# Optimization experiments

Hardware: AMD Instinct MI355X
Metric: run time of the kernel (lower is better)

Reference implementation:

```python
import jax, jax.numpy as jnp
import numpy as np

B, N, DIM, EMB_H, EXP, K = 1, 1024, 64, 64, 4, 16


def setup_inputs() -> dict:
    key = jax.random.key(0)
    ks = jax.random.split(key, 12)
    s = lambda k, *shape: jax.random.normal(k, shape, dtype=jnp.float32) * 0.05
    return {
        "x": jax.random.normal(ks[0], (B, N, DIM), dtype=jnp.float32),
        "pos": jax.random.normal(ks[1], (B, N, 3), dtype=jnp.float32),
        "Wq": s(ks[2], DIM, DIM),
        "Wk": s(ks[3], DIM, DIM),
        "Wv": s(ks[4], DIM, DIM),
        "P1": s(ks[5], 3, EMB_H), "pb1": jnp.zeros((EMB_H,), jnp.float32),
        "P2": s(ks[6], EMB_H, DIM), "pb2": jnp.zeros((DIM,), jnp.float32),
        "A1": s(ks[7], DIM, DIM * EXP), "ab1": jnp.zeros((DIM * EXP,), jnp.float32),
        "A2": s(ks[8], DIM * EXP, DIM), "ab2": jnp.zeros((DIM,), jnp.float32),
        "nneighbors": K,
    }


def reference(x, pos, Wq, Wk, Wv, P1, pb1, P2, pb2, A1, ab1, A2, ab2, nneighbors):
    b, n, d = x.shape
    q = x @ Wq            # [b,n,d]
    k = x @ Wk
    v = x @ Wv
    qk_rel = q[:, :, None, :] - k[:, None, :, :]          # [b,n,n,d]
    rel_pos = pos[:, :, None, :] - pos[:, None, :, :]      # [b,n,n,3]
    rel_pos_emb = jax.nn.relu(rel_pos @ P1 + pb1) @ P2 + pb2  # [b,n,n,d]
    # kNN selection on euclidean distance (smallest nneighbors)
    rel_dist = jnp.linalg.norm(rel_pos, axis=-1)           # [b,n,n]
    _, idx = jax.lax.top_k(-rel_dist, nneighbors)          # [b,n,K]
    bidx = jnp.arange(b)[:, None, None]
    v_g = v[bidx, idx]                                     # [b,n,K,d]
    qk_g = jnp.take_along_axis(qk_rel, idx[..., None], axis=2)        # [b,n,K,d]
    rpe_g = jnp.take_along_axis(rel_pos_emb, idx[..., None], axis=2)  # [b,n,K,d]
    v_g = v_g + rpe_g
    sim = jax.nn.relu((qk_g + rpe_g) @ A1 + ab1) @ A2 + ab2  # [b,n,K,d]
    attn = jax.nn.softmax(sim, axis=-2)                      # softmax over neighbors
    agg = jnp.sum(attn * v_g, axis=2)                        # [b,n,d]
    return agg
```

## Files before the change

kernel.cpp:

```cpp
#include <hip/hip_runtime.h>
#include <climits>

#define NPTS 1024
#define DIMD 64
#define KNN  16
#define HID  256
#define EMBH 64

typedef short short8 __attribute__((ext_vector_type(8)));
typedef float f32x4  __attribute__((ext_vector_type(4)));

__device__ __forceinline__ short f2bf(float x) {
    unsigned u = __float_as_uint(x);
    unsigned r = (u + 0x7fffu + ((u >> 16) & 1u)) >> 16;
    return (short)r;
}
__device__ __forceinline__ float bf2f(short s) {
    return __uint_as_float(((unsigned)(unsigned short)s) << 16);
}

#define AOFF(k, m) ((((k) >> 3) * 16 + (m)) * 8 + ((k) & 7))

#define A1H 0
#define A2H 16384
#define WKH 32768
#define WVH 36864
#define P2H 40960

__global__ __launch_bounds__(256) void prep_weights(
    const float* __restrict__ A1, const float* __restrict__ A2,
    const float* __restrict__ Wk, const float* __restrict__ Wv,
    const float* __restrict__ P2, short* __restrict__ ws)
{
    int e = blockIdx.x * 256 + threadIdx.x;
    if (e >= 88 * 64) return;
    int f = e >> 6, lane = e & 63;
    int q = (lane >> 4) & 3, nn = lane & 15;
    const float* src; int N, base, lf, cpt;
    if (f < 32)      { src = A1; N = 256; base = A1H; lf = f;      cpt = 2; }
    else if (f < 64) { src = A2; N = 64;  base = A2H; lf = f - 32; cpt = 8; }
    else if (f < 72) { src = Wk; N = 64;  base = WKH; lf = f - 64; cpt = 2; }
    else if (f < 80) { src = Wv; N = 64;  base = WVH; lf = f - 72; cpt = 2; }
    else             { src = P2; N = 64;  base = P2H; lf = f - 80; cpt = 2; }
    int T = lf / cpt, c = lf % cpt;
    int n  = T * 16 + nn;
    int k0 = c * 32 + q * 8;
    short8 v;
    #pragma unroll
    for (int j = 0; j < 8; j++) v[j] = f2bf(src[(k0 + j) * N + n]);
    *(short8*)(ws + base + lf * 512 + lane * 8) = v;
}

__global__ __launch_bounds__(256, 4) void ptl_fused(
    const float* __restrict__ x,  const float* __restrict__ pos,
    const float* __restrict__ Wq,
    const float* __restrict__ P1, const float* __restrict__ pb1,
    const float* __restrict__ pb2,
    const float* __restrict__ ab1, const float* __restrict__ ab2,
    const short* __restrict__ ws,
    float* __restrict__ out)
{
    __shared__ __align__(16) short a_xn_hi[16*64],  a_xn_lo[16*64];
    __shared__ __align__(16) short a_es_hi[16*64],  a_es_lo[16*64];
    __shared__ __align__(16) short a_h_hi [16*64],  a_h_lo [16*64];
    __shared__ __align__(16) short a_hd[2*16*256];
    __shared__ __align__(16) float s_vg[16*68];
    __shared__ __align__(16) float s_sim[16*68];
    __shared__ float s_q[DIMD];
    __shared__ int   s_idx[KNN];
    __shared__ int   s_cnt, s_cnt2, s_need;
    __shared__ unsigned s_pref;

    short* a_hd_hi = a_hd;
    short* a_hd_lo = a_hd + 16*256;

    const int i    = blockIdx.x;
    const int tid  = threadIdx.x;
    const int lane = tid & 63;
    const int w    = tid >> 6;
    const int q4   = lane >> 4;
    const int col  = lane & 15;

    const float px = pos[i*3+0], py = pos[i*3+1], pz = pos[i*3+2];

    unsigned ku[4];
    #pragma unroll
    for (int u = 0; u < 4; u++) {
        int j = tid + 256 * u;
        float dx = __fsub_rn(px, pos[j*3+0]);
        float dy = __fsub_rn(py, pos[j*3+1]);
        float dz = __fsub_rn(pz, pos[j*3+2]);
        float s  = __fadd_rn(__fadd_rn(__fmul_rn(dx,dx), __fmul_rn(dy,dy)), __fmul_rn(dz,dz));
        ku[u] = __float_as_uint(__fsqrt_rn(s));
    }

    int* histI = (int*)a_hd;
    int* s_tie = (int*)(a_hd + 16*256);
    const int g = w * 4 + q4;
    if (tid == 0) { s_cnt = 0; s_cnt2 = 0; s_pref = 0u; s_need = KNN; }

    for (int r = 0; r < 4; r++) {
        const int shift = 24 - 8 * r;
        for (int t = tid; t < 16 * 256; t += 256) histI[t] = 0;
        __syncthreads();
        unsigned pref = s_pref;
        #pragma unroll
        for (int u = 0; u < 4; u++) {
            unsigned k = ku[u];
            bool match = true;
            if (r > 0) match = ((k >> (shift + 8)) == (pref >> (shift + 8)));
            if (match) atomicAdd(&histI[g * 256 + ((k >> shift) & 255)], 1);
        }
        __syncthreads();
        if (w == 0) {
            int b0 = lane * 4, cnt4[4], loc = 0;
            #pragma unroll
            for (int t = 0; t < 4; t++) {
                int s = 0;
                #pragma unroll
                for (int gg = 0; gg < 16; gg++) s += histI[gg * 256 + b0 + t];
                cnt4[t] = s; loc += s;
            }
            int incl = loc;
            #pragma unroll
            for (int off = 1; off < 64; off <<= 1) {
                int t = __shfl_up(incl, off);
                if (lane >= off) incl += t;
            }
            int excl = incl - loc;
            int need = s_need;
            unsigned long long mk = __ballot(incl >= need);
            int lstar = (int)__ffsll((long long)mk) - 1;
            if (lane == lstar) {
                int run = excl, t = 0;
                while (t < 3 && run + cnt4[t] < need) { run += cnt4[t]; t++; }
                s_pref = pref | ((unsigned)(b0 + t) << shift);
                s_need = need - run;
            }
        }
        __syncthreads();
    }
    const unsigned T = s_pref;
    const int needT  = s_need;

    #pragma unroll
    for (int u = 0; u < 4; u++) {
        unsigned k = ku[u];
        int j = tid + 256 * u;
        if (k < T)       { int p = atomicAdd(&s_cnt, 1);  s_idx[p] = j; }
        else if (k == T) { int p = atomicAdd(&s_cnt2, 1); if (p < 256) s_tie[p] = j; }
    }
    __syncthreads();

    if (w == 0) {
        int base = s_cnt;
        int m = s_cnt2;
        if (m == needT) {
            for (int t = lane; t < m; t += 64) s_idx[base + t] = s_tie[t];
        } else {
            int cand[4];
            #pragma unroll
            for (int t = 0; t < 4; t++) {
                int e = lane + 64 * t;
                cand[t] = (e < m && e < 256) ? s_tie[e] : INT_MAX;
            }
            for (int sel = 0; sel < needT; sel++) {
                int mv = cand[0];
                #pragma unroll
                for (int t = 1; t < 4; t++) mv = min(mv, cand[t]);
                #pragma unroll
                for (int off = 32; off > 0; off >>= 1) mv = min(mv, __shfl_xor(mv, off));
                #pragma unroll
                for (int t = 0; t < 4; t++) if (cand[t] == mv) cand[t] = INT_MAX;
                if (lane == 0) s_idx[base + sel] = mv;
            }
        }
    } else if (w == 1) {
        int d = lane;
        const float4* xr = (const float4*)(x + i * DIMD);
        float aq = 0.f;
        #pragma unroll
        for (int cb = 0; cb < DIMD / 4; cb++) {
            float4 xv = xr[cb];
            const float* wq = Wq + (cb*4) * DIMD + d;
            aq = fmaf(xv.x, wq[0*DIMD], aq); aq = fmaf(xv.y, wq[1*DIMD], aq);
            aq = fmaf(xv.z, wq[2*DIMD], aq); aq = fmaf(xv.w, wq[3*DIMD], aq);
        }
        s_q[d] = aq;
    }
    __syncthreads();

    #pragma unroll
    for (int u = 0; u < 4; u++) {
        int t = tid + 256 * u;
        int kk = t >> 6, c = t & 63;
        int j = s_idx[kk];
        int ao = AOFF(c, kk);
        float xv = x[j * DIMD + c];
        short xh = f2bf(xv);
        a_xn_hi[ao] = xh;
        a_xn_lo[ao] = f2bf(xv - bf2f(xh));
        float dx = px - pos[j*3+0];
        float dy = py - pos[j*3+1];
        float dz = pz - pos[j*3+2];
        float a = pb1[c];
        a = fmaf(dx, P1[0*EMBH+c], a);
        a = fmaf(dy, P1[1*EMBH+c], a);
        a = fmaf(dz, P1[2*EMBH+c], a);
        a = fmaxf(a, 0.0f);
        short eh = f2bf(a);
        a_es_hi[ao] = eh;
        a_es_lo[ao] = f2bf(a - bf2f(eh));
    }
    __syncthreads();

    const short8* wsv  = (const short8*)ws;
    const short8* xnh  = (const short8*)a_xn_hi;
    const short8* xnl  = (const short8*)a_xn_lo;
    const short8* esh  = (const short8*)a_es_hi;
    const short8* esl  = (const short8*)a_es_lo;
    const short8* hhv  = (const short8*)a_h_hi;
    const short8* hlv  = (const short8*)a_h_lo;
    const short8* hdh  = (const short8*)a_hd_hi;
    const short8* hdl  = (const short8*)a_hd_lo;

    auto bfrag = [&](int short_base, int f) -> short8 {
        return wsv[(short_base >> 3) + f * 64 + lane];
    };

    {
        f32x4 acck = {0,0,0,0}, accv = {0,0,0,0}, accr = {0,0,0,0};
        #pragma unroll
        for (int c = 0; c < 2; c++) {
            int av = (4*c + q4) * 16 + col;
            short8 xh = xnh[av], xl = xnl[av];
            int f = w * 2 + c;
            short8 bk = bfrag(WKH, f);
            short8 bv = bfrag(WVH, f);
            acck = __builtin_amdgcn_mfma_f32_16x16x32_bf16(xh, bk, acck, 0,0,0);
            acck = __builtin_amdgcn_mfma_f32_16x16x32_bf16(xl, bk, acck, 0,0,0);
            accv = __builtin_amdgcn_mfma_f32_16x16x32_bf16(xh, bv, accv, 0,0,0);
            accv = __builtin_amdgcn_mfma_f32_16x16x32_bf16(xl, bv, accv, 0,0,0);
        }
        #pragma unroll
        for (int c = 0; c < 2; c++) {
            int av = (4*c + q4) * 16 + col;
            short8 eh = esh[av], el = esl[av];
            short8 bp = bfrag(P2H, w * 2 + c);
            accr = __builtin_amdgcn_mfma_f32_16x16x32_bf16(eh, bp, accr, 0,0,0);
            accr = __builtin_amdgcn_mfma_f32_16x16x32_bf16(el, bp, accr, 0,0,0);
        }
        int d = w * 16 + col;
        float qd = s_q[d], pb = pb2[d];
        #pragma unroll
        for (int r = 0; r < 4; r++) {
            int s = q4 * 4 + r;
            float rpe = accr[r] + pb;
            float hv  = qd - acck[r] + rpe;
            s_vg[s * 68 + d] = accv[r] + rpe;
            int ao = AOFF(d, s);
            short hh = f2bf(hv);
            a_h_hi[ao] = hh;
            a_h_lo[ao] = f2bf(hv - bf2f(hh));
        }
    }
    __syncthreads();

    {
        short8 hh[2], hl[2];
        #pragma unroll
        for (int c = 0; c < 2; c++) {
            int av = (4*c + q4) * 16 + col;
            hh[c] = hhv[av]; hl[c] = hlv[av];
        }
        #pragma unroll
        for (int t = 0; t < 4; t++) {
            int T4 = w * 4 + t;
            f32x4 acc = {0,0,0,0};
            #pragma unroll
            for (int c = 0; c < 2; c++) {
                short8 bh = bfrag(A1H, T4 * 2 + c);
                acc = __builtin_amdgcn_mfma_f32_16x16x32_bf16(hh[c], bh, acc, 0,0,0);
                acc = __builtin_amdgcn_mfma_f32_16x16x32_bf16(hl[c], bh, acc, 0,0,0);
            }
            int n = T4 * 16 + col;
            float bias = ab1[n];
            #pragma unroll
            for (int r = 0; r < 4; r++) {
                float val = fmaxf(acc[r] + bias, 0.0f);
                int ao = AOFF(n, q4 * 4 + r);
                short vh = f2bf(val);
                a_hd_hi[ao] = vh;
                a_hd_lo[ao] = f2bf(val - bf2f(vh));
            }
        }
    }
    __syncthreads();

    {
        f32x4 acc0 = {0,0,0,0}, acc1 = {0,0,0,0};
        #pragma unroll
        for (int c = 0; c < 8; c += 2) {
            {
                int av = (4*c + q4) * 16 + col;
                short8 ah = hdh[av], al = hdl[av];
                short8 bh = bfrag(A2H, w * 8 + c);
                acc0 = __builtin_amdgcn_mfma_f32_16x16x32_bf16(ah, bh, acc0, 0,0,0);
                acc0 = __builtin_amdgcn_mfma_f32_16x16x32_bf16(al, bh, acc0, 0,0,0);
            }
            {
                int av = (4*(c+1) + q4) * 16 + col;
                short8 ah = hdh[av], al = hdl[av];
                short8 bh = bfrag(A2H, w * 8 + c + 1);
                acc1 = __builtin_amdgcn_mfma_f32_16x16x32_bf16(ah, bh, acc1, 0,0,0);
                acc1 = __builtin_amdgcn_mfma_f32_16x16x32_bf16(al, bh, acc1, 0,0,0);
            }
        }
        int n = w * 16 + col;
        float bias = ab2[n];
        #pragma unroll
        for (int r = 0; r < 4; r++)
            s_sim[(q4 * 4 + r) * 68 + n] = acc0[r] + acc1[r] + bias;
    }
    __syncthreads();

    if (tid < DIMD) {
        int d = tid;
        float mx = -3.0e38f;
        #pragma unroll
        for (int kk = 0; kk < KNN; kk++) mx = fmaxf(mx, s_sim[kk * 68 + d]);
        float den = 0.0f, num = 0.0f;
        #pragma unroll
        for (int kk = 0; kk < KNN; kk++) {
            float e = expf(s_sim[kk * 68 + d] - mx);
            den += e;
            num = fmaf(e, s_vg[kk * 68 + d], num);
        }
        out[i * DIMD + d] = num / den;
    }
}

extern "C" void kernel_launch(void* const* d_in, const int* in_sizes, int n_in,
                              void* d_out, int out_size, void* d_ws, size_t ws_size,
                              hipStream_t stream) {
    const float* x   = (const float*)d_in[0];
    const float* pos = (const float*)d_in[1];
    const float* Wq  = (const float*)d_in[2];
    const float* Wk  = (const float*)d_in[3];
    const float* Wv  = (const float*)d_in[4];
    const float* P1  = (const float*)d_in[5];
    const float* pb1 = (const float*)d_in[6];
    const float* P2  = (const float*)d_in[7];
    const float* pb2 = (const float*)d_in[8];
    const float* A1  = (const float*)d_in[9];
    const float* ab1 = (const float*)d_in[10];
    const float* A2  = (const float*)d_in[11];
    const float* ab2 = (const float*)d_in[12];
    float* out = (float*)d_out;
    short* ws  = (short*)d_ws;

    prep_weights<<<22, 256, 0, stream>>>(A1, A2, Wk, Wv, P2, ws);
    ptl_fused<<<NPTS, 256, 0, stream>>>(x, pos, Wq, P1, pb1, pb2, ab1, ab2, ws, out);
}
```

Measured before the change: 97.36 us.

## Drop bf16 hi/lo split and redo radix-select with per-wave double-buffered histograms

Activations are now rounded once to bf16 instead of being split into hi and lo parts, which halves the MFMA count and the LDS traffic for the A operands in every GEMM stage. The kNN radix select now uses four per-wave histograms in double-buffered LDS. Every wave does the scan redundantly and shares prefix and need through shuffles instead of shared variables, which removes one barrier per round and the full histogram clear. The cost is lower activation precision, so outputs may drift further from the fp32 reference.

```diff
diff --git a/kernel.cpp b/kernel.cpp
--- a/kernel.cpp
+++ b/kernel.cpp
@@ -14,9 +14,6 @@
     unsigned u = __float_as_uint(x);
     unsigned r = (u + 0x7fffu + ((u >> 16) & 1u)) >> 16;
     return (short)r;
-}
-__device__ __forceinline__ float bf2f(short s) {
-    return __uint_as_float(((unsigned)(unsigned short)s) << 16);
 }
 
 #define AOFF(k, m) ((((k) >> 3) * 16 + (m)) * 8 + ((k) & 7))
@@ -60,19 +57,17 @@
     const short* __restrict__ ws,
     float* __restrict__ out)
 {
-    __shared__ __align__(16) short a_xn_hi[16*64],  a_xn_lo[16*64];
-    __shared__ __align__(16) short a_es_hi[16*64],  a_es_lo[16*64];
-    __shared__ __align__(16) short a_h_hi [16*64],  a_h_lo [16*64];
-    __shared__ __align__(16) short a_hd[2*16*256];
+    __shared__ __align__(16) short a_xn[16*64];
+    __shared__ __align__(16) short a_es[16*64];
+    __shared__ __align__(16) short a_h [16*64];
+    __shared__ __align__(16) short a_hd[16*256];
     __shared__ __align__(16) float s_vg[16*68];
     __shared__ __align__(16) float s_sim[16*68];
     __shared__ float s_q[DIMD];
+    __shared__ int   s_hist[2 * 1028];
+    __shared__ int   s_tie[256];
     __shared__ int   s_idx[KNN];
-    __shared__ int   s_cnt, s_cnt2, s_need;
-    __shared__ unsigned s_pref;
-
-    short* a_hd_hi = a_hd;
-    short* a_hd_lo = a_hd + 16*256;
+    __shared__ int   s_cnt, s_cnt2;
 
     const int i    = blockIdx.x;
     const int tid  = threadIdx.x;
@@ -80,6 +75,9 @@
     const int w    = tid >> 6;
     const int q4   = lane >> 4;
     const int col  = lane & 15;
+
+    int* histA = s_hist;
+    int* histB = s_hist + 1028;
 
     const float px = pos[i*3+0], py = pos[i*3+1], pz = pos[i*3+2];
 
@@ -93,55 +91,51 @@
         float s  = __fadd_rn(__fadd_rn(__fmul_rn(dx,dx), __fmul_rn(dy,dy)), __fmul_rn(dz,dz));
         ku[u] = __float_as_uint(__fsqrt_rn(s));
     }
-
-    int* histI = (int*)a_hd;
-    int* s_tie = (int*)(a_hd + 16*256);
-    const int g = w * 4 + q4;
-    if (tid == 0) { s_cnt = 0; s_cnt2 = 0; s_pref = 0u; s_need = KNN; }
-
+    if (tid == 0) { s_cnt = 0; s_cnt2 = 0; }
+    for (int t = lane; t < 257; t += 64) { histA[w*257 + t] = 0; histB[w*257 + t] = 0; }
+    __syncthreads();
+
+    unsigned pref = 0u; int need = KNN;
     for (int r = 0; r < 4; r++) {
         const int shift = 24 - 8 * r;
-        for (int t = tid; t < 16 * 256; t += 256) histI[t] = 0;
-        __syncthreads();
-        unsigned pref = s_pref;
+        int* cur = (r & 1) ? histB : histA;
         #pragma unroll
         for (int u = 0; u < 4; u++) {
             unsigned k = ku[u];
-            bool match = true;
-            if (r > 0) match = ((k >> (shift + 8)) == (pref >> (shift + 8)));
-            if (match) atomicAdd(&histI[g * 256 + ((k >> shift) & 255)], 1);
+            bool match = (r == 0) || ((k >> (shift + 8)) == (pref >> (shift + 8)));
+            if (match) atomicAdd(&cur[w * 257 + ((k >> shift) & 255)], 1);
         }
         __syncthreads();
-        if (w == 0) {
-            int b0 = lane * 4, cnt4[4], loc = 0;
+        int b0 = lane * 4, cnt4[4], loc = 0;
+        #pragma unroll
+        for (int t = 0; t < 4; t++) {
+            int s = 0;
             #pragma unroll
-            for (int t = 0; t < 4; t++) {
-                int s = 0;
-                #pragma unroll
-                for (int gg = 0; gg < 16; gg++) s += histI[gg * 256 + b0 + t];
-                cnt4[t] = s; loc += s;
-            }
-            int incl = loc;
-            #pragma unroll
-            for (int off = 1; off < 64; off <<= 1) {
-                int t = __shfl_up(incl, off);
-                if (lane >= off) incl += t;
-            }
-            int excl = incl - loc;
-            int need = s_need;
-            unsigned long long mk = __ballot(incl >= need);
-            int lstar = (int)__ffsll((long long)mk) - 1;
-            if (lane == lstar) {
-                int run = excl, t = 0;
-                while (t < 3 && run + cnt4[t] < need) { run += cnt4[t]; t++; }
-                s_pref = pref | ((unsigned)(b0 + t) << shift);
-                s_need = need - run;
-            }
-        }
-        __syncthreads();
-    }
-    const unsigned T = s_pref;
-    const int needT  = s_need;
+            for (int ww = 0; ww < 4; ww++) s += cur[ww * 257 + b0 + t];
+            cnt4[t] = s; loc += s;
+        }
+        int incl = loc;
+        #pragma unroll
+        for (int off = 1; off < 64; off <<= 1) {
+            int t = __shfl_up(incl, off);
+            if (lane >= off) incl += t;
+        }
+        int excl = incl - loc;
+        unsigned long long mk = __ballot(incl >= need);
+        int lstar = (int)__ffsll((long long)mk) - 1;
+        int run = excl, t = 0;
+        while (t < 3 && run + cnt4[t] < need) { run += cnt4[t]; t++; }
+        unsigned cand_pref = pref | ((unsigned)(b0 + t) << shift);
+        int cand_need = need - run;
+        pref = (unsigned)__shfl((int)cand_pref, lstar);
+        need = __shfl(cand_need, lstar);
+        if (r == 1 || r == 2) {
+            int* oth = (r & 1) ? histA : histB;
+            for (int tt = lane; tt < 257; tt += 64) oth[w*257 + tt] = 0;
+        }
+    }
+    const unsigned T = pref;
+    const int needT  = need;
 
     #pragma unroll
     for (int u = 0; u < 4; u++) {
@@ -196,10 +190,7 @@
         int kk = t >> 6, c = t & 63;
         int j = s_idx[kk];
         int ao = AOFF(c, kk);
-        float xv = x[j * DIMD + c];
-        short xh = f2bf(xv);
-        a_xn_hi[ao] = xh;
-        a_xn_lo[ao] = f2bf(xv - bf2f(xh));
+        a_xn[ao] = f2bf(x[j * DIMD + c]);
         float dx = px - pos[j*3+0];
         float dy = py - pos[j*3+1];
         float dz = pz - pos[j*3+2];
@@ -207,22 +198,15 @@
         a = fmaf(dx, P1[0*EMBH+c], a);
         a = fmaf(dy, P1[1*EMBH+c], a);
         a = fmaf(dz, P1[2*EMBH+c], a);
-        a = fmaxf(a, 0.0f);
-        short eh = f2bf(a);
-        a_es_hi[ao] = eh;
-        a_es_lo[ao] = f2bf(a - bf2f(eh));
-    }
-    __syncthreads();
-
-    const short8* wsv  = (const short8*)ws;
-    const short8* xnh  = (const short8*)a_xn_hi;
-    const short8* xnl  = (const short8*)a_xn_lo;
-    const short8* esh  = (const short8*)a_es_hi;
-    const short8* esl  = (const short8*)a_es_lo;
-    const short8* hhv  = (const short8*)a_h_hi;
-    const short8* hlv  = (const short8*)a_h_lo;
-    const short8* hdh  = (const short8*)a_hd_hi;
-    const short8* hdl  = (const short8*)a_hd_lo;
+        a_es[ao] = f2bf(fmaxf(a, 0.0f));
+    }
+    __syncthreads();
+
+    const short8* wsv = (const short8*)ws;
+    const short8* xnv = (const short8*)a_xn;
+    const short8* esv = (const short8*)a_es;
+    const short8* hv_ = (const short8*)a_h;
+    const short8* hdv = (const short8*)a_hd;
 
     auto bfrag = [&](int short_base, int f) -> short8 {
         return wsv[(short_base >> 3) + f * 64 + lane];
@@ -233,22 +217,14 @@
         #pragma unroll
         for (int c = 0; c < 2; c++) {
             int av = (4*c + q4) * 16 + col;
-            short8 xh = xnh[av], xl = xnl[av];
+            short8 xh = xnv[av], eh = esv[av];
             int f = w * 2 + c;
             short8 bk = bfrag(WKH, f);
             short8 bv = bfrag(WVH, f);
+            short8 bp = bfrag(P2H, f);
             acck = __builtin_amdgcn_mfma_f32_16x16x32_bf16(xh, bk, acck, 0,0,0);
-            acck = __builtin_amdgcn_mfma_f32_16x16x32_bf16(xl, bk, acck, 0,0,0);
             accv = __builtin_amdgcn_mfma_f32_16x16x32_bf16(xh, bv, accv, 0,0,0);
-            accv = __builtin_amdgcn_mfma_f32_16x16x32_bf16(xl, bv, accv, 0,0,0);
-        }
-        #pragma unroll
-        for (int c = 0; c < 2; c++) {
-            int av = (4*c + q4) * 16 + col;
-            short8 eh = esh[av], el = esl[av];
-            short8 bp = bfrag(P2H, w * 2 + c);
             accr = __builtin_amdgcn_mfma_f32_16x16x32_bf16(eh, bp, accr, 0,0,0);
-            accr = __builtin_amdgcn_mfma_f32_16x16x32_bf16(el, bp, accr, 0,0,0);
         }
         int d = w * 16 + col;
         float qd = s_q[d], pb = pb2[d];
@@ -258,20 +234,17 @@
             float rpe = accr[r] + pb;
             float hv  = qd - acck[r] + rpe;
             s_vg[s * 68 + d] = accv[r] + rpe;
-            int ao = AOFF(d, s);
-            short hh = f2bf(hv);
-            a_h_hi[ao] = hh;
-            a_h_lo[ao] = f2bf(hv - bf2f(hh));
+            a_h[AOFF(d, s)] = f2bf(hv);
         }
     }
     __syncthreads();
 
     {
-        short8 hh[2], hl[2];
+        short8 hh[2];
         #pragma unroll
         for (int c = 0; c < 2; c++) {
             int av = (4*c + q4) * 16 + col;
-            hh[c] = hhv[av]; hl[c] = hlv[av];
+            hh[c] = hv_[av];
         }
         #pragma unroll
         for (int t = 0; t < 4; t++) {
@@ -281,17 +254,13 @@
             for (int c = 0; c < 2; c++) {
                 short8 bh = bfrag(A1H, T4 * 2 + c);
                 acc = __builtin_amdgcn_mfma_f32_16x16x32_bf16(hh[c], bh, acc, 0,0,0);
-                acc = __builtin_amdgcn_mfma_f32_16x16x32_bf16(hl[c], bh, acc, 0,0,0);
             }
             int n = T4 * 16 + col;
             float bias = ab1[n];
             #pragma unroll
             for (int r = 0; r < 4; r++) {
                 float val = fmaxf(acc[r] + bias, 0.0f);
-                int ao = AOFF(n, q4 * 4 + r);
-                short vh = f2bf(val);
-                a_hd_hi[ao] = vh;
-                a_hd_lo[ao] = f2bf(val - bf2f(vh));
+                a_hd[AOFF(n, q4 * 4 + r)] = f2bf(val);
             }
         }
     }
@@ -303,17 +272,15 @@
         for (int c = 0; c < 8; c += 2) {
             {
                 int av = (4*c + q4) * 16 + col;
-                short8 ah = hdh[av], al = hdl[av];
+                short8 ah = hdv[av];
                 short8 bh = bfrag(A2H, w * 8 + c);
                 acc0 = __builtin_amdgcn_mfma_f32_16x16x32_bf16(ah, bh, acc0, 0,0,0);
-                acc0 = __builtin_amdgcn_mfma_f32_16x16x32_bf16(al, bh, acc0, 0,0,0);
             }
             {
                 int av = (4*(c+1) + q4) * 16 + col;
-                short8 ah = hdh[av], al = hdl[av];
+                short8 ah = hdv[av];
                 short8 bh = bfrag(A2H, w * 8 + c + 1);
                 acc1 = __builtin_amdgcn_mfma_f32_16x16x32_bf16(ah, bh, acc1, 0,0,0);
-                acc1 = __builtin_amdgcn_mfma_f32_16x16x32_bf16(al, bh, acc1, 0,0,0);
             }
         }
         int n = w * 16 + col;
```

After: 94.56 us. -2.9%, faster.
